# Kernel tuning notes

Measured on AMD Instinct MI355X. Metric: run time of the kernel, lower is better.

## Reference

```python
import jax, jax.numpy as jnp
import numpy as np

B, SQ, SKV, E, H = 4, 2048, 2048, 1024, 16
D = E // H  # head_dim = 64


def setup_inputs() -> dict:
    key = jax.random.key(0)
    ks = jax.random.split(key, 8)
    s = 1.0 / np.sqrt(D)
    return {
        "query": jax.random.normal(ks[0], (B, SQ, E), jnp.float32),
        "key_value": jax.random.normal(ks[1], (B, SKV, E), jnp.float32),
        "wq": jax.random.normal(ks[2], (H, D, D), jnp.float32) * s,
        "bq": jnp.zeros((H, D), jnp.float32),
        "wk": jax.random.normal(ks[3], (H, D, D), jnp.float32) * s,
        "bk": jnp.zeros((H, D), jnp.float32),
        "wv": jax.random.normal(ks[4], (H, D, D), jnp.float32) * s,
        "bv": jnp.zeros((H, D), jnp.float32),
        "wo": jax.random.normal(ks[5], (E, E), jnp.float32) * (1.0 / np.sqrt(E)),
        "bo": jnp.zeros((E,), jnp.float32),
    }


def reference(query, key_value, wq, bq, wk, bk, wv, bv, wo, bo):
    b, sq, e = query.shape
    skv = key_value.shape[1]
    h, d = wq.shape[0], wq.shape[1]
    # split into heads: [B, S, H, D]
    q = query.reshape(b, sq, h, d)
    kv = key_value.reshape(b, skv, h, d)
    # per-head Linear projections (torch Linear: y = x @ W^T + b), batched over H
    qh = jnp.einsum('bshd,hed->bshe', q, wq) + bq   # [B,Sq,H,D]
    kh = jnp.einsum('bthd,hed->bthe', kv, wk) + bk  # [B,Skv,H,D]
    vh = jnp.einsum('bthd,hed->bthe', kv, wv) + bv  # [B,Skv,H,D]
    # scaled dot-product cross attention per head
    scores = jnp.einsum('bshd,bthd->bhst', qh, kh) / jnp.sqrt(jnp.asarray(d, qh.dtype))
    attn = jax.nn.softmax(scores, axis=-1)          # [B,H,Sq,Skv]
    ctx = jnp.einsum('bhst,bthd->bshd', attn, vh)   # [B,Sq,H,D]
    # concat heads then output projection W_O
    out = ctx.reshape(b, sq, e)
    return out @ wo.T + bo
```

## Files before the change

kernel.cpp:

```cpp
#include <hip/hip_runtime.h>

#define B_ 4
#define SQ_ 2048
#define SKV_ 2048
#define E_ 1024
#define H_ 16
#define D_ 64

typedef __bf16 bf16x8 __attribute__((ext_vector_type(8)));
typedef __bf16 bf16x4 __attribute__((ext_vector_type(4)));
typedef float f32x4 __attribute__((ext_vector_type(4)));

__device__ inline f32x4 zero4() { f32x4 z = {0.f, 0.f, 0.f, 0.f}; return z; }

__device__ inline bf16x8 cvt8(const float* __restrict__ p) {
    const float4 a = ((const float4*)p)[0];
    const float4 b = ((const float4*)p)[1];
    bf16x8 r;
    r[0] = (__bf16)a.x; r[1] = (__bf16)a.y; r[2] = (__bf16)a.z; r[3] = (__bf16)a.w;
    r[4] = (__bf16)b.x; r[5] = (__bf16)b.y; r[6] = (__bf16)b.z; r[7] = (__bf16)b.w;
    return r;
}

#define MFMA16(a, b, c) __builtin_amdgcn_mfma_f32_16x16x32_bf16(a, b, c, 0, 0, 0)

#define QSCALE 0.18033688011112042f

__device__ inline void stage16(const __bf16* g, __bf16* l) {
    __builtin_amdgcn_global_load_lds(
        (const __attribute__((address_space(1))) void*)g,
        (__attribute__((address_space(3))) void*)l, 16, 0, 0);
}

__global__ __launch_bounds__(256) void cast_wo_kernel(const float* __restrict__ wo,
                                                      __bf16* __restrict__ wo_bf) {
    int i = (blockIdx.x * 256 + threadIdx.x) * 4;
    float4 v = *(const float4*)(wo + i);
    wo_bf[i + 0] = (__bf16)v.x;
    wo_bf[i + 1] = (__bf16)v.y;
    wo_bf[i + 2] = (__bf16)v.z;
    wo_bf[i + 3] = (__bf16)v.w;
}

__global__ __launch_bounds__(256) void proj_q_kernel(const float* __restrict__ q,
                                                     const float* __restrict__ wq,
                                                     const float* __restrict__ bq,
                                                     __bf16* __restrict__ qh) {
    __shared__ __bf16 tile[64 * 72];
    const int w = threadIdx.x >> 6, lane = threadIdx.x & 63;
    const int l15 = lane & 15, quad = lane >> 4;
    const int b = blockIdx.z, h = blockIdx.y;
    const int s_blk = blockIdx.x * 64;
    const int s_base = s_blk + w * 16;

    const float* qrow = q + ((size_t)b * SQ_ + s_base + l15) * E_ + h * D_ + quad * 8;
    bf16x8 a0 = cvt8(qrow);
    bf16x8 a1 = cvt8(qrow + 32);

    f32x4 acc[4] = {zero4(), zero4(), zero4(), zero4()};
#pragma unroll
    for (int nb = 0; nb < 4; ++nb) {
        const float* wrow = wq + (size_t)h * D_ * D_ + (nb * 16 + l15) * D_ + quad * 8;
        bf16x8 b0 = cvt8(wrow);
        bf16x8 b1 = cvt8(wrow + 32);
        acc[nb] = MFMA16(a0, b0, acc[nb]);
        acc[nb] = MFMA16(a1, b1, acc[nb]);
    }

#pragma unroll
    for (int nb = 0; nb < 4; ++nb) {
        const int col = nb * 16 + l15;
        const float bias = bq[h * D_ + col];
#pragma unroll
        for (int r = 0; r < 4; ++r) {
            tile[(w * 16 + quad * 4 + r) * 72 + col] =
                (__bf16)((acc[nb][r] + bias) * QSCALE);
        }
    }
    __syncthreads();

    __bf16* obase = qh + ((size_t)(b * H_ + h) * SQ_ + s_blk) * D_;
    const int tid = threadIdx.x;
#pragma unroll
    for (int i = 0; i < 2; ++i) {
        const int seg = i * 256 + tid;
        const int row = seg >> 3, sg = seg & 7;
        bf16x8 v = *(const bf16x8*)&tile[row * 72 + sg * 8];
        *(bf16x8*)&obase[(size_t)row * D_ + sg * 8] = v;
    }
}

__global__ __launch_bounds__(256) void proj_kv_kernel(const float* __restrict__ kv,
                                                      const float* __restrict__ wk,
                                                      const float* __restrict__ bk,
                                                      const float* __restrict__ wv,
                                                      const float* __restrict__ bv,
                                                      __bf16* __restrict__ kh,
                                                      __bf16* __restrict__ vh) {
    __shared__ __bf16 ktile[64 * 72];
    __shared__ __bf16 vtile[64 * 72];
    const int w = threadIdx.x >> 6, lane = threadIdx.x & 63;
    const int l15 = lane & 15, quad = lane >> 4;
    const int b = blockIdx.z, h = blockIdx.y;
    const int t_base = blockIdx.x * 64 + w * 16;

    const float* xrow = kv + ((size_t)b * SKV_ + t_base + l15) * E_ + h * D_ + quad * 8;
    bf16x8 a0 = cvt8(xrow);
    bf16x8 a1 = cvt8(xrow + 32);

    f32x4 acck[4] = {zero4(), zero4(), zero4(), zero4()};
    f32x4 accv[4] = {zero4(), zero4(), zero4(), zero4()};
#pragma unroll
    for (int nb = 0; nb < 4; ++nb) {
        const float* wkrow = wk + (size_t)h * D_ * D_ + (nb * 16 + l15) * D_ + quad * 8;
        const float* wvrow = wv + (size_t)h * D_ * D_ + (nb * 16 + l15) * D_ + quad * 8;
        bf16x8 bk0 = cvt8(wkrow);
        bf16x8 bk1 = cvt8(wkrow + 32);
        bf16x8 bv0 = cvt8(wvrow);
        bf16x8 bv1 = cvt8(wvrow + 32);
        acck[nb] = MFMA16(a0, bk0, acck[nb]);
        acck[nb] = MFMA16(a1, bk1, acck[nb]);
        accv[nb] = MFMA16(a0, bv0, accv[nb]);
        accv[nb] = MFMA16(a1, bv1, accv[nb]);
    }

#pragma unroll
    for (int nb = 0; nb < 4; ++nb) {
        const int col = nb * 16 + l15;
        const float biask = bk[h * D_ + col];
        const float biasv = bv[h * D_ + col];
#pragma unroll
        for (int r = 0; r < 4; ++r) {
            const int row = quad * 4 + r;
            const int tl = w * 16 + row;
            const int kcol = (((col >> 3) ^ (row & 7)) << 3) | (col & 7);
            ktile[tl * 72 + kcol] = (__bf16)(acck[nb][r] + biask);
            const int vcol = (((tl >> 3) ^ (col & 7)) << 3) | (tl & 7);
            vtile[col * 72 + vcol] = (__bf16)(accv[nb][r] + biasv);
        }
    }
    __syncthreads();

    const int bh = b * H_ + h;
    __bf16* kbase = kh + ((size_t)bh * SKV_ + blockIdx.x * 64) * D_;
    __bf16* vbase = vh + (((size_t)bh * (SKV_ / 64) + blockIdx.x) * 64) * 64;
    const int tid = threadIdx.x;
#pragma unroll
    for (int i = 0; i < 2; ++i) {
        const int seg = i * 256 + tid;
        const int row = seg >> 3, sg = seg & 7;
        bf16x8 kv8 = *(const bf16x8*)&ktile[row * 72 + sg * 8];
        *(bf16x8*)&kbase[(size_t)row * D_ + sg * 8] = kv8;
        bf16x8 vv8 = *(const bf16x8*)&vtile[row * 72 + sg * 8];
        *(bf16x8*)&vbase[(size_t)row * 64 + sg * 8] = vv8;
    }
}

__global__ __launch_bounds__(256, 2) void attn_kernel(const __bf16* __restrict__ qh,
                                                      const __bf16* __restrict__ kh,
                                                      const __bf16* __restrict__ vh,
                                                      __bf16* __restrict__ ctx) {
    __shared__ __bf16 k_lds[2][4096];
    __shared__ __bf16 v_lds[2][4096];
    __shared__ __bf16 t_lds[4][16][72];

    const int w = threadIdx.x >> 6, lane = threadIdx.x & 63;
    const int l15 = lane & 15, quad = lane >> 4;
    const int f = blockIdx.x;
    const int g = f & 63, tq = f >> 6;
    const int b = g >> 4, h = g & 15;
    const int bh = b * H_ + h;
    const int s_base = tq * 256 + w * 64;
    const int sw8 = (l15 & 7) << 3;

    bf16x8 aq[4][2];
#pragma unroll
    for (int qt = 0; qt < 4; ++qt) {
        const __bf16* qb = qh + ((size_t)bh * SQ_ + s_base + qt * 16 + l15) * D_ + quad * 8;
        aq[qt][0] = *(const bf16x8*)qb;
        aq[qt][1] = *(const bf16x8*)(qb + 32);
    }

    const __bf16 one_bf = (__bf16)1.0f;
    bf16x8 ones;
#pragma unroll
    for (int j = 0; j < 8; ++j) ones[j] = one_bf;

    f32x4 oT[4][4];
    f32x4 lacc[4];
#pragma unroll
    for (int qt = 0; qt < 4; ++qt) {
        lacc[qt] = zero4();
#pragma unroll
        for (int db = 0; db < 4; ++db) oT[qt][db] = zero4();
    }

    const __bf16* kt = kh + (size_t)bh * SKV_ * D_;
    const __bf16* vt = vh + (size_t)bh * SKV_ * D_;

    auto stage = [&](int buf, int it) {
#pragma unroll
        for (int c2 = 0; c2 < 2; ++c2) {
            const int c = w + c2 * 4;
            stage16(kt + (size_t)it * 4096 + c * 512 + lane * 8, &k_lds[buf][c * 512]);
            stage16(vt + (size_t)it * 4096 + c * 512 + lane * 8, &v_lds[buf][c * 512]);
        }
    };

    stage(0, 0);
    __syncthreads();

    for (int it = 0; it < SKV_ / 64; ++it) {
        const int cur = it & 1;
        if (it + 1 < SKV_ / 64) stage(cur ^ 1, it + 1);

        bf16x8 kf0[4], kf1[4];
#pragma unroll
        for (int nb = 0; nb < 4; ++nb) {
            const __bf16* kr = &k_lds[cur][(nb * 16 + l15) * 64];
            kf0[nb] = *(const bf16x8*)&kr[(quad << 3) ^ sw8];
            kf1[nb] = *(const bf16x8*)&kr[((quad + 4) << 3) ^ sw8];
        }
        bf16x8 vtf[4][2];
#pragma unroll
        for (int db = 0; db < 4; ++db) {
            const __bf16* vr = &v_lds[cur][(db * 16 + l15) * 64];
#pragma unroll
            for (int a = 0; a < 2; ++a) {
                const int c_lo = a * 4 + (quad >> 1);
                const int lo_off = (((c_lo ^ (l15 & 7)) << 3) | ((quad & 1) * 4));
                const int hi_off = ((((c_lo + 2) ^ (l15 & 7)) << 3) | ((quad & 1) * 4));
                union { bf16x8 v8; bf16x4 h2[2]; } u;
                u.h2[0] = *(const bf16x4*)&vr[lo_off];
                u.h2[1] = *(const bf16x4*)&vr[hi_off];
                vtf[db][a] = u.v8;
            }
        }
#pragma unroll
        for (int qt = 0; qt < 4; ++qt) {
            f32x4 s[4] = {zero4(), zero4(), zero4(), zero4()};
#pragma unroll
            for (int nb = 0; nb < 4; ++nb) {
                s[nb] = MFMA16(kf0[nb], aq[qt][0], s[nb]);
                s[nb] = MFMA16(kf1[nb], aq[qt][1], s[nb]);
            }
            bf16x8 pb[2];
#pragma unroll
            for (int a = 0; a < 2; ++a) {
#pragma unroll
                for (int hf = 0; hf < 2; ++hf) {
                    const int nb = a * 2 + hf;
                    pb[a][hf * 4 + 0] = (__bf16)__builtin_amdgcn_exp2f(s[nb][0]);
                    pb[a][hf * 4 + 1] = (__bf16)__builtin_amdgcn_exp2f(s[nb][1]);
                    pb[a][hf * 4 + 2] = (__bf16)__builtin_amdgcn_exp2f(s[nb][2]);
                    pb[a][hf * 4 + 3] = (__bf16)__builtin_amdgcn_exp2f(s[nb][3]);
                }
            }
            lacc[qt] = MFMA16(ones, pb[0], lacc[qt]);
            lacc[qt] = MFMA16(ones, pb[1], lacc[qt]);
#pragma unroll
            for (int db = 0; db < 4; ++db)
#pragma unroll
                for (int a = 0; a < 2; ++a)
                    oT[qt][db] = MFMA16(vtf[db][a], pb[a], oT[qt][db]);
        }
        __syncthreads();
    }

#pragma unroll
    for (int qt = 0; qt < 4; ++qt) {
        const float inv = 1.f / lacc[qt][0];
#pragma unroll
        for (int db = 0; db < 4; ++db) {
#pragma unroll
            for (int r = 0; r < 4; ++r) {
                t_lds[w][l15][db * 16 + quad * 4 + r] = (__bf16)(oT[qt][db][r] * inv);
            }
        }
#pragma unroll
        for (int pp = 0; pp < 2; ++pp) {
            const int row = (lane >> 3) + pp * 8;
            bf16x8 vrow = *(const bf16x8*)&t_lds[w][row][(lane & 7) * 8];
            *(bf16x8*)&ctx[((size_t)b * SQ_ + s_base + qt * 16 + row) * E_ + h * D_ +
                           (lane & 7) * 8] = vrow;
        }
    }
}

__global__ __launch_bounds__(256, 2) void ogemm_kernel(const __bf16* __restrict__ ctx,
                                                       const __bf16* __restrict__ wo_bf,
                                                       const float* __restrict__ bo,
                                                       float* __restrict__ out) {
    __shared__ __bf16 a_lds[2][8192];
    __shared__ __bf16 b_lds[2][8192];

    const int w = threadIdx.x >> 6, lane = threadIdx.x & 63;
    const int l15 = lane & 15, quad = lane >> 4;
    const int f = blockIdx.x;
    const int mblk = f & 63, nblk = f >> 6;
    const int m0 = mblk * 128, n0 = nblk * 128;
    const int wm = (w >> 1) * 64, wn = (w & 1) * 64;

    f32x4 acc[4][4];
#pragma unroll
    for (int sub = 0; sub < 4; ++sub)
#pragma unroll
        for (int nb = 0; nb < 4; ++nb) acc[sub][nb] = zero4();

    const int sr = lane >> 3, sc = lane & 7;
    auto stage = [&](int buf, int kk) {
#pragma unroll
        for (int i = 0; i < 4; ++i) {
            const int c = w * 4 + i;
            const int r = c * 8 + sr;
            const int col8 = sc ^ (r & 7);
            stage16(ctx + (size_t)(m0 + r) * E_ + kk + col8 * 8, &a_lds[buf][c * 512]);
            stage16(wo_bf + (size_t)(n0 + r) * E_ + kk + col8 * 8, &b_lds[buf][c * 512]);
        }
    };

    stage(0, 0);
    __syncthreads();

    for (int it = 0; it < E_ / 64; ++it) {
        const int cur = it & 1;
        if (it + 1 < E_ / 64) stage(cur ^ 1, (it + 1) * 64);

#pragma unroll
        for (int h = 0; h < 2; ++h) {
            bf16x8 af[4], bf[4];
            const int cq = ((h * 4 + quad) ^ (l15 & 7)) * 8;
#pragma unroll
            for (int sub = 0; sub < 4; ++sub)
                af[sub] = *(const bf16x8*)&a_lds[cur][(wm + sub * 16 + l15) * 64 + cq];
#pragma unroll
            for (int nb = 0; nb < 4; ++nb)
                bf[nb] = *(const bf16x8*)&b_lds[cur][(wn + nb * 16 + l15) * 64 + cq];
#pragma unroll
            for (int nb = 0; nb < 4; ++nb)
#pragma unroll
                for (int sub = 0; sub < 4; ++sub)
                    acc[sub][nb] = MFMA16(af[sub], bf[nb], acc[sub][nb]);
        }
        __syncthreads();
    }

#pragma unroll
    for (int sub = 0; sub < 4; ++sub) {
#pragma unroll
        for (int nb = 0; nb < 4; ++nb) {
            const int col = n0 + wn + nb * 16 + l15;
            const float bias = bo[col];
#pragma unroll
            for (int r = 0; r < 4; ++r) {
                const int row = m0 + wm + sub * 16 + quad * 4 + r;
                out[(size_t)row * E_ + col] = acc[sub][nb][r] + bias;
            }
        }
    }
}

extern "C" void kernel_launch(void* const* d_in, const int* in_sizes, int n_in,
                              void* d_out, int out_size, void* d_ws, size_t ws_size,
                              hipStream_t stream) {
    const float* query = (const float*)d_in[0];
    const float* key_value = (const float*)d_in[1];
    const float* wq = (const float*)d_in[2];
    const float* bq = (const float*)d_in[3];
    const float* wk = (const float*)d_in[4];
    const float* bk = (const float*)d_in[5];
    const float* wv = (const float*)d_in[6];
    const float* bv = (const float*)d_in[7];
    const float* wo = (const float*)d_in[8];
    const float* bo = (const float*)d_in[9];
    float* out = (float*)d_out;

    char* ws = (char*)d_ws;
    __bf16* qh = (__bf16*)(ws);
    __bf16* kh = (__bf16*)(ws + (16u << 20));
    __bf16* vh = (__bf16*)(ws + (32u << 20));
    __bf16* ctxb = (__bf16*)(ws + (48u << 20));
    __bf16* wo_bf = (__bf16*)(ws + (64u << 20));

    hipLaunchKernelGGL(cast_wo_kernel, dim3(E_ * E_ / 1024), dim3(256), 0, stream, wo, wo_bf);
    hipLaunchKernelGGL(proj_q_kernel, dim3(SQ_ / 64, H_, B_), dim3(256), 0, stream,
                       query, wq, bq, qh);
    hipLaunchKernelGGL(proj_kv_kernel, dim3(SKV_ / 64, H_, B_), dim3(256), 0, stream,
                       key_value, wk, bk, wv, bv, kh, vh);
    hipLaunchKernelGGL(attn_kernel, dim3(B_ * H_ * (SQ_ / 256)), dim3(256), 0, stream,
                       qh, kh, vh, ctxb);
    hipLaunchKernelGGL(ogemm_kernel, dim3((B_ * SQ_ / 128) * (E_ / 128)), dim3(256), 0, stream,
                       ctxb, wo_bf, bo, out);
}
```

Measured before the change: 253.6 us.

## Fuse Q projection into attention and merge KV projection with Wo cast

The Q projection now runs inside the attention kernel. Each wave reads fp32 query rows, runs the projection with MFMA and round-trips the result through its LDS scratch tile to get the A-operand layout, so the bf16 qh buffer is no longer written and re-read. The Wo cast and the K/V projection are merged into one prep kernel, cutting five launches to three. The cost is extra fp32 loads and MFMA work at the start of each attention block, plus possible LDS hazards on the reused t_lds tile if per-wave ordering is not guaranteed.

Result: faster. 234.7 us, median of 2 (-7.4%).

```diff
diff --git a/kernel.cpp b/kernel.cpp
--- a/kernel.cpp
+++ b/kernel.cpp
@@ -32,77 +32,33 @@
         (__attribute__((address_space(3))) void*)l, 16, 0, 0);
 }
 
-__global__ __launch_bounds__(256) void cast_wo_kernel(const float* __restrict__ wo,
-                                                      __bf16* __restrict__ wo_bf) {
-    int i = (blockIdx.x * 256 + threadIdx.x) * 4;
-    float4 v = *(const float4*)(wo + i);
-    wo_bf[i + 0] = (__bf16)v.x;
-    wo_bf[i + 1] = (__bf16)v.y;
-    wo_bf[i + 2] = (__bf16)v.z;
-    wo_bf[i + 3] = (__bf16)v.w;
-}
-
-__global__ __launch_bounds__(256) void proj_q_kernel(const float* __restrict__ q,
-                                                     const float* __restrict__ wq,
-                                                     const float* __restrict__ bq,
-                                                     __bf16* __restrict__ qh) {
-    __shared__ __bf16 tile[64 * 72];
+__global__ __launch_bounds__(256) void prep_kernel(const float* __restrict__ kv,
+                                                   const float* __restrict__ wk,
+                                                   const float* __restrict__ bk,
+                                                   const float* __restrict__ wv,
+                                                   const float* __restrict__ bv,
+                                                   const float* __restrict__ wo,
+                                                   __bf16* __restrict__ kh,
+                                                   __bf16* __restrict__ vh,
+                                                   __bf16* __restrict__ wo_bf) {
+    __shared__ __bf16 ktile[64 * 72];
+    __shared__ __bf16 vtile[64 * 72];
+
+    if (blockIdx.x < 1024) {
+        int i = (blockIdx.x * 256 + threadIdx.x) * 4;
+        float4 v = *(const float4*)(wo + i);
+        wo_bf[i + 0] = (__bf16)v.x;
+        wo_bf[i + 1] = (__bf16)v.y;
+        wo_bf[i + 2] = (__bf16)v.z;
+        wo_bf[i + 3] = (__bf16)v.w;
+        return;
+    }
+
+    const int bx = blockIdx.x - 1024;
+    const int sblk = bx & 31, h = (bx >> 5) & 15, b = bx >> 9;
     const int w = threadIdx.x >> 6, lane = threadIdx.x & 63;
     const int l15 = lane & 15, quad = lane >> 4;
-    const int b = blockIdx.z, h = blockIdx.y;
-    const int s_blk = blockIdx.x * 64;
-    const int s_base = s_blk + w * 16;
-
-    const float* qrow = q + ((size_t)b * SQ_ + s_base + l15) * E_ + h * D_ + quad * 8;
-    bf16x8 a0 = cvt8(qrow);
-    bf16x8 a1 = cvt8(qrow + 32);
-
-    f32x4 acc[4] = {zero4(), zero4(), zero4(), zero4()};
-#pragma unroll
-    for (int nb = 0; nb < 4; ++nb) {
-        const float* wrow = wq + (size_t)h * D_ * D_ + (nb * 16 + l15) * D_ + quad * 8;
-        bf16x8 b0 = cvt8(wrow);
-        bf16x8 b1 = cvt8(wrow + 32);
-        acc[nb] = MFMA16(a0, b0, acc[nb]);
-        acc[nb] = MFMA16(a1, b1, acc[nb]);
-    }
-
-#pragma unroll
-    for (int nb = 0; nb < 4; ++nb) {
-        const int col = nb * 16 + l15;
-        const float bias = bq[h * D_ + col];
-#pragma unroll
-        for (int r = 0; r < 4; ++r) {
-            tile[(w * 16 + quad * 4 + r) * 72 + col] =
-                (__bf16)((acc[nb][r] + bias) * QSCALE);
-        }
-    }
-    __syncthreads();
-
-    __bf16* obase = qh + ((size_t)(b * H_ + h) * SQ_ + s_blk) * D_;
-    const int tid = threadIdx.x;
-#pragma unroll
-    for (int i = 0; i < 2; ++i) {
-        const int seg = i * 256 + tid;
-        const int row = seg >> 3, sg = seg & 7;
-        bf16x8 v = *(const bf16x8*)&tile[row * 72 + sg * 8];
-        *(bf16x8*)&obase[(size_t)row * D_ + sg * 8] = v;
-    }
-}
-
-__global__ __launch_bounds__(256) void proj_kv_kernel(const float* __restrict__ kv,
-                                                      const float* __restrict__ wk,
-                                                      const float* __restrict__ bk,
-                                                      const float* __restrict__ wv,
-                                                      const float* __restrict__ bv,
-                                                      __bf16* __restrict__ kh,
-                                                      __bf16* __restrict__ vh) {
-    __shared__ __bf16 ktile[64 * 72];
-    __shared__ __bf16 vtile[64 * 72];
-    const int w = threadIdx.x >> 6, lane = threadIdx.x & 63;
-    const int l15 = lane & 15, quad = lane >> 4;
-    const int b = blockIdx.z, h = blockIdx.y;
-    const int t_base = blockIdx.x * 64 + w * 16;
+    const int t_base = sblk * 64 + w * 16;
 
     const float* xrow = kv + ((size_t)b * SKV_ + t_base + l15) * E_ + h * D_ + quad * 8;
     bf16x8 a0 = cvt8(xrow);
@@ -142,8 +98,8 @@
     __syncthreads();
 
     const int bh = b * H_ + h;
-    __bf16* kbase = kh + ((size_t)bh * SKV_ + blockIdx.x * 64) * D_;
-    __bf16* vbase = vh + (((size_t)bh * (SKV_ / 64) + blockIdx.x) * 64) * 64;
+    __bf16* kbase = kh + ((size_t)bh * SKV_ + sblk * 64) * D_;
+    __bf16* vbase = vh + (((size_t)bh * (SKV_ / 64) + sblk) * 64) * 64;
     const int tid = threadIdx.x;
 #pragma unroll
     for (int i = 0; i < 2; ++i) {
@@ -156,7 +112,9 @@
     }
 }
 
-__global__ __launch_bounds__(256, 2) void attn_kernel(const __bf16* __restrict__ qh,
+__global__ __launch_bounds__(256, 2) void attn_kernel(const float* __restrict__ q,
+                                                      const float* __restrict__ wq,
+                                                      const float* __restrict__ bq,
                                                       const __bf16* __restrict__ kh,
                                                       const __bf16* __restrict__ vh,
                                                       __bf16* __restrict__ ctx) {
@@ -174,11 +132,38 @@
     const int sw8 = (l15 & 7) << 3;
 
     bf16x8 aq[4][2];
-#pragma unroll
-    for (int qt = 0; qt < 4; ++qt) {
-        const __bf16* qb = qh + ((size_t)bh * SQ_ + s_base + qt * 16 + l15) * D_ + quad * 8;
-        aq[qt][0] = *(const bf16x8*)qb;
-        aq[qt][1] = *(const bf16x8*)(qb + 32);
+    {
+        __bf16* twp = &t_lds[w][0][0];
+        bf16x8 bw[4][2];
+#pragma unroll
+        for (int nb = 0; nb < 4; ++nb) {
+            const float* wrow = wq + (size_t)h * D_ * D_ + (nb * 16 + l15) * D_ + quad * 8;
+            bw[nb][0] = cvt8(wrow);
+            bw[nb][1] = cvt8(wrow + 32);
+        }
+#pragma unroll
+        for (int qt = 0; qt < 4; ++qt) {
+            const float* qrow =
+                q + ((size_t)b * SQ_ + s_base + qt * 16 + l15) * E_ + h * D_ + quad * 8;
+            bf16x8 a0 = cvt8(qrow);
+            bf16x8 a1 = cvt8(qrow + 32);
+            f32x4 acc[4] = {zero4(), zero4(), zero4(), zero4()};
+#pragma unroll
+            for (int nb = 0; nb < 4; ++nb) {
+                acc[nb] = MFMA16(a0, bw[nb][0], acc[nb]);
+                acc[nb] = MFMA16(a1, bw[nb][1], acc[nb]);
+            }
+#pragma unroll
+            for (int nb = 0; nb < 4; ++nb) {
+                const int col = nb * 16 + l15;
+                const float bias = bq[h * D_ + col];
+#pragma unroll
+                for (int r = 0; r < 4; ++r)
+                    twp[(quad * 4 + r) * 72 + col] = (__bf16)((acc[nb][r] + bias) * QSCALE);
+            }
+            aq[qt][0] = *(const bf16x8*)&twp[l15 * 72 + quad * 8];
+            aq[qt][1] = *(const bf16x8*)&twp[l15 * 72 + 32 + quad * 8];
+        }
     }
 
     const __bf16 one_bf = (__bf16)1.0f;
@@ -376,19 +361,15 @@
     float* out = (float*)d_out;
 
     char* ws = (char*)d_ws;
-    __bf16* qh = (__bf16*)(ws);
-    __bf16* kh = (__bf16*)(ws + (16u << 20));
-    __bf16* vh = (__bf16*)(ws + (32u << 20));
-    __bf16* ctxb = (__bf16*)(ws + (48u << 20));
-    __bf16* wo_bf = (__bf16*)(ws + (64u << 20));
-
-    hipLaunchKernelGGL(cast_wo_kernel, dim3(E_ * E_ / 1024), dim3(256), 0, stream, wo, wo_bf);
-    hipLaunchKernelGGL(proj_q_kernel, dim3(SQ_ / 64, H_, B_), dim3(256), 0, stream,
-                       query, wq, bq, qh);
-    hipLaunchKernelGGL(proj_kv_kernel, dim3(SKV_ / 64, H_, B_), dim3(256), 0, stream,
-                       key_value, wk, bk, wv, bv, kh, vh);
+    __bf16* kh = (__bf16*)(ws);
+    __bf16* vh = (__bf16*)(ws + (16u << 20));
+    __bf16* ctxb = (__bf16*)(ws + (32u << 20));
+    __bf16* wo_bf = (__bf16*)(ws + (48u << 20));
+
+    hipLaunchKernelGGL(prep_kernel, dim3(1024 + B_ * H_ * (SKV_ / 64)), dim3(256), 0, stream,
+                       key_value, wk, bk, wv, bv, wo, kh, vh, wo_bf);
     hipLaunchKernelGGL(attn_kernel, dim3(B_ * H_ * (SQ_ / 256)), dim3(256), 0, stream,
-                       qh, kh, vh, ctxb);
+                       query, wq, bq, kh, vh, ctxb);
     hipLaunchKernelGGL(ogemm_kernel, dim3((B_ * SQ_ / 128) * (E_ / 128)), dim3(256), 0, stream,
                        ctxb, wo_bf, bo, out);
 }
```
